# Kernel optimization log

Measured on AMD Instinct MI355X. Metric: run time of the kernel, lower is better.

## Reference

```python
import jax, jax.numpy as jnp
from jax import lax
import numpy as np

B, C, H, W = 32, 64, 128, 128
O, K, KS = 64, 4, 3
HIDDEN = int(C * 0.25) + 1  # 17, per ScaleAwareAttention2d


def setup_inputs() -> dict:
    key = jax.random.key(0)
    ks = jax.random.split(key, 6)
    return {
        "x": jax.random.normal(ks[0], (B, C, H, W), dtype=jnp.float32),
        "scale": jax.random.uniform(ks[1], (1,), dtype=jnp.float32),
        "fc1_w": jax.random.normal(ks[2], (HIDDEN, C), dtype=jnp.float32) * 0.1,
        "fc2_w": jax.random.normal(ks[3], (K, HIDDEN + 2), dtype=jnp.float32) * 0.1,
        "fc2_b": jnp.zeros((K,), dtype=jnp.float32),
        "weight": jax.random.normal(ks[4], (K, O, C, KS, KS), dtype=jnp.float32) * 0.05,
        "bias": jax.random.normal(ks[5], (K, O), dtype=jnp.float32) * 0.05,
    }


def reference(x, scale, fc1_w, fc2_w, fc2_b, weight, bias):
    b = x.shape[0]
    # --- ScaleAwareAttention2d (eval mode -> temperature = 1) ---
    pooled = x.mean(axis=(2, 3))                      # [B, C]  (adaptive avg pool to 1x1)
    h = jax.nn.relu(pooled @ fc1_w.T)                 # [B, HIDDEN]  (1x1 conv, no bias)
    h = jnp.concatenate([h, jnp.ones((b, 2), x.dtype) * scale], axis=1)  # [B, HIDDEN+2]
    logits = h @ fc2_w.T + fc2_b                      # [B, K]
    attn = jax.nn.softmax(logits, axis=1)             # temperature = 1 at inference

    # --- per-sample weight/bias aggregation ---
    agg_w = jnp.einsum('bk,koihw->boihw', attn, weight)  # [B, O, C, KS, KS]
    agg_b = attn @ bias                                   # [B, O]

    # --- per-sample conv (equivalent of F.conv2d with groups = batch) ---
    def one_sample(xi, wi):
        return lax.conv_general_dilated(
            xi[None], wi, window_strides=(1, 1), padding=((1, 1), (1, 1)),
            dimension_numbers=('NCHW', 'OIHW', 'NCHW'))[0]

    out = jax.vmap(one_sample)(x, agg_w)              # [B, O, H, W]
    return out + agg_b[:, :, None, None]
```

## Files before the change

kernel.cpp:

```cpp
#include <hip/hip_runtime.h>
#include <hip/hip_bf16.h>

#define BB 32
#define CC 64
#define HH 128
#define WW 128
#define OO 64
#define KK 4
#define HIDDEN 17
#define HW (HH*WW)

typedef __attribute__((ext_vector_type(8)))  short bf16x8;
typedef __attribute__((ext_vector_type(16))) float f32x16;

typedef __attribute__((address_space(3))) void       lds_void_t;
typedef const __attribute__((address_space(1))) void gbl_void_t;

__device__ __forceinline__ unsigned short f2bf(float f) {
    unsigned u = __float_as_uint(f);
    unsigned r = (u + 0x7FFFu + ((u >> 16) & 1u)) >> 16;
    return (unsigned short)r;
}

__global__ __launch_bounds__(256) void zero_pool_kernel(float* __restrict__ pooled) {
    int i = blockIdx.x * 256 + threadIdx.x;
    if (i < BB * CC) pooled[i] = 0.f;
}

__global__ __launch_bounds__(256) void pool_kernel(const float* __restrict__ x,
                                                   float* __restrict__ pooled) {
    int bc = blockIdx.x;
    const float* p = x + (size_t)bc * HW;
    float s = 0.f;
    for (int i = threadIdx.x; i < HW; i += 256) s += p[i];
    #pragma unroll
    for (int off = 32; off > 0; off >>= 1) s += __shfl_down(s, off, 64);
    __shared__ float warp_s[4];
    int lane = threadIdx.x & 63, wv = threadIdx.x >> 6;
    if (lane == 0) warp_s[wv] = s;
    __syncthreads();
    if (threadIdx.x == 0) {
        float t = warp_s[0] + warp_s[1] + warp_s[2] + warp_s[3];
        pooled[bc] = t * (1.f / (float)HW);
    }
}

__global__ __launch_bounds__(256) void attn_kernel(const float* __restrict__ pooled,
                                                   const float* __restrict__ fc1_w,
                                                   const float* __restrict__ fc2_w,
                                                   const float* __restrict__ fc2_b,
                                                   const float* __restrict__ scale,
                                                   const float* __restrict__ bias,
                                                   float* __restrict__ attn,
                                                   float* __restrict__ agg_b) {
    __shared__ float s_attn[BB * KK];
    int tid = threadIdx.x;
    if (tid < BB) {
        int b = tid;
        const float* pb = pooled + b * CC;
        float h[HIDDEN];
        #pragma unroll
        for (int i = 0; i < HIDDEN; ++i) {
            float s = 0.f;
            for (int c = 0; c < CC; ++c) s += pb[c] * fc1_w[i * CC + c];
            h[i] = fmaxf(s, 0.f);
        }
        float sc = scale[0];
        float logits[KK];
        #pragma unroll
        for (int k = 0; k < KK; ++k) {
            float s = fc2_b[k];
            for (int j = 0; j < HIDDEN; ++j) s += h[j] * fc2_w[k * (HIDDEN + 2) + j];
            s += sc * fc2_w[k * (HIDDEN + 2) + HIDDEN];
            s += sc * fc2_w[k * (HIDDEN + 2) + HIDDEN + 1];
            logits[k] = s;
        }
        float m = fmaxf(fmaxf(logits[0], logits[1]), fmaxf(logits[2], logits[3]));
        float e[KK], tot = 0.f;
        #pragma unroll
        for (int k = 0; k < KK; ++k) { e[k] = __expf(logits[k] - m); tot += e[k]; }
        float inv = 1.f / tot;
        #pragma unroll
        for (int k = 0; k < KK; ++k) {
            float a = e[k] * inv;
            s_attn[b * KK + k] = a;
            attn[b * KK + k] = a;
        }
    }
    __syncthreads();
    for (int i = tid; i < BB * OO; i += blockDim.x) {
        int b = i >> 6;
        int o = i & 63;
        float s = 0.f;
        #pragma unroll
        for (int k = 0; k < KK; ++k) s += s_attn[b * KK + k] * bias[k * OO + o];
        agg_b[i] = s;
    }
}

__global__ __launch_bounds__(256) void aggw_fused_kernel(const float* __restrict__ pooled,
                                                         const float* __restrict__ fc1_w,
                                                         const float* __restrict__ fc2_w,
                                                         const float* __restrict__ fc2_b,
                                                         const float* __restrict__ scale,
                                                         const float* __restrict__ bias,
                                                         const float* __restrict__ weight,
                                                         float* __restrict__ agg_b,
                                                         unsigned int* __restrict__ wbf) {
    __shared__ float4 sw4[128 * 37];
    __shared__ float  sh[4][20];
    __shared__ float  sa[4][4];
    const float* swf = (const float*)sw4;

    const int tid = threadIdx.x;
    const int b4  = blockIdx.x;
    const int oty = blockIdx.y;
    const int kcz = blockIdx.z;

    {
        const float4* w4 = (const float4*)weight;
        #pragma unroll
        for (int it = 0; it < 18; ++it) {
            int i   = tid + it * 256;
            int seg = i / 36;
            int off = i - seg * 36;
            int k   = seg >> 5;
            int o   = seg & 31;
            sw4[seg * 37 + off] = w4[(size_t)(k * 64 + oty * 32 + o) * 144 + kcz * 36 + off];
        }
    }
    const int wv = tid >> 6, lane = tid & 63;
    const int bb = b4 * 4 + wv;
    if (lane < HIDDEN) {
        const float* pb = pooled + bb * CC;
        const float* f1 = fc1_w + lane * CC;
        float s = 0.f;
        #pragma unroll
        for (int c = 0; c < CC; ++c) s += pb[c] * f1[c];
        sh[wv][lane] = fmaxf(s, 0.f);
    }
    __syncthreads();
    if (lane == 0) {
        float sc = scale[0];
        float lg[KK];
        #pragma unroll
        for (int k = 0; k < KK; ++k) {
            float s = fc2_b[k];
            #pragma unroll
            for (int j = 0; j < HIDDEN; ++j) s += sh[wv][j] * fc2_w[k * (HIDDEN + 2) + j];
            s += sc * fc2_w[k * (HIDDEN + 2) + HIDDEN];
            s += sc * fc2_w[k * (HIDDEN + 2) + HIDDEN + 1];
            lg[k] = s;
        }
        float m = fmaxf(fmaxf(lg[0], lg[1]), fmaxf(lg[2], lg[3]));
        float e[KK], tot = 0.f;
        #pragma unroll
        for (int k = 0; k < KK; ++k) { e[k] = __expf(lg[k] - m); tot += e[k]; }
        float inv = 1.f / tot;
        #pragma unroll
        for (int k = 0; k < KK; ++k) sa[wv][k] = e[k] * inv;
    }
    __syncthreads();

    if (oty == 0 && kcz == 0) {
        int bl = tid >> 6, o = tid & 63;
        float s = 0.f;
        #pragma unroll
        for (int k = 0; k < KK; ++k) s += sa[bl][k] * bias[k * OO + o];
        agg_b[(b4 * 4 + bl) * OO + o] = s;
    }

    const int lane6 = tid >> 2;
    const int j2    = tid & 3;
    const int m     = lane6 & 31;
    const int kh2   = lane6 >> 5;
    const int cl    = kh2 * 8 + j2 * 2;
    #pragma unroll
    for (int bl = 0; bl < 4; ++bl) {
        const int b = b4 * 4 + bl;
        const float a0 = sa[bl][0], a1 = sa[bl][1], a2 = sa[bl][2], a3 = sa[bl][3];
        #pragma unroll
        for (int j9 = 0; j9 < 9; ++j9) {
            float s0, s1;
            {
                const float* p0 = swf + (0 * 32 + m) * 148 + cl * 9 + j9;
                const float* p1 = swf + (1 * 32 + m) * 148 + cl * 9 + j9;
                const float* p2 = swf + (2 * 32 + m) * 148 + cl * 9 + j9;
                const float* p3 = swf + (3 * 32 + m) * 148 + cl * 9 + j9;
                s0 = a0 * p0[0] + a1 * p1[0] + a2 * p2[0] + a3 * p3[0];
                s1 = a0 * p0[9] + a1 * p1[9] + a2 * p2[9] + a3 * p3[9];
            }
            wbf[(((size_t)b * 9 + j9) * 8 + oty * 4 + kcz) * 256 + tid] =
                (unsigned int)f2bf(s0) | ((unsigned int)f2bf(s1) << 16);
        }
    }
}

__global__ __launch_bounds__(256) void xpose_pool_kernel(const float* __restrict__ x,
                                                         unsigned int* __restrict__ xbf32,
                                                         float* __restrict__ pooled) {
    __shared__ float t2[64][68];
    __shared__ float s_red[4][64];
    const int y  = blockIdx.x;
    const int b  = blockIdx.y;
    const int x0 = blockIdx.z * 64;
    const int tid = threadIdx.x;
    {
        const int xq = tid & 15;
        const int cb = (tid >> 4) * 4;
        #pragma unroll
        for (int i = 0; i < 4; ++i) {
            const int c = cb + i;
            const float4 v = *(const float4*)(x + (size_t)(b * CC + c) * HW
                                                + (size_t)y * WW + x0 + xq * 4);
            t2[xq * 4 + 0][c] = v.x;
            t2[xq * 4 + 1][c] = v.y;
            t2[xq * 4 + 2][c] = v.z;
            t2[xq * 4 + 3][c] = v.w;
        }
    }
    __syncthreads();
    {
        const int c = tid & 63, q = tid >> 6;
        float s = 0.f;
        #pragma unroll
        for (int i = 0; i < 16; ++i) s += t2[q * 16 + i][c];
        s_red[q][c] = s;
    }
    {
        const int xl  = tid >> 2;
        const int xg  = x0 + xl;
        const int key = (xg + 1) & 7;
        unsigned int* dst = xbf32 + ((size_t)(b * HH + y) * WW + xg) * 32;
        #pragma unroll
        for (int gg = 0; gg < 2; ++gg) {
            const int g = (tid & 3) + gg * 4;
            const float* src = &t2[xl][g * 8];
            uint4 pk;
            pk.x = (unsigned int)f2bf(src[0]) | ((unsigned int)f2bf(src[1]) << 16);
            pk.y = (unsigned int)f2bf(src[2]) | ((unsigned int)f2bf(src[3]) << 16);
            pk.z = (unsigned int)f2bf(src[4]) | ((unsigned int)f2bf(src[5]) << 16);
            pk.w = (unsigned int)f2bf(src[6]) | ((unsigned int)f2bf(src[7]) << 16);
            *(uint4*)(dst + (g ^ key) * 4) = pk;
        }
    }
    __syncthreads();
    if (tid < CC) {
        float s = s_red[0][tid] + s_red[1][tid] + s_red[2][tid] + s_red[3][tid];
        atomicAdd(pooled + b * CC + tid, s * (1.f / (float)HW));
    }
}

#define LROW 16640
__global__ __launch_bounds__(256, 3) void conv_mfma_kernel(const short* __restrict__ xbf,
                                                           const short* __restrict__ wbf,
                                                           const float* __restrict__ agg_b,
                                                           float* __restrict__ out) {
    __shared__ __attribute__((aligned(16))) char ldsbuf[3 * LROW];
    unsigned int* lds32 = (unsigned int*)ldsbuf;

    const int s    = blockIdx.x;
    const int y    = ((s & 7) << 4) | (s >> 3);
    const int b    = blockIdx.y;
    const int tid  = threadIdx.x;
    const int lane = tid & 63;
    const int w    = tid >> 6;

    if (tid < 192) {
        int r = tid / 64;
        int q = tid - r * 64;
        int word = (q < 32) ? (r * (LROW/4) + q)
                            : (r * (LROW/4) + 129 * 32 + (q - 32));
        lds32[word] = 0u;
    }
    {
        const short* growb = xbf + (size_t)b * HH * WW * CC;
        #pragma unroll
        for (int i = 0; i < 12; ++i) {
            int call = w * 12 + i;
            int r   = call >> 4;
            int seg = call & 15;
            int iy  = y - 1 + r;
            if (iy >= 0 && iy < HH) {
                const short* g = growb + (size_t)iy * (WW * CC) + seg * 512 + lane * 8;
                char* lp = ldsbuf + r * LROW + 128 + seg * 1024;
                __builtin_amdgcn_global_load_lds((gbl_void_t*)g, (lds_void_t*)lp, 16, 0, 0);
            }
        }
    }
    if (y == 0)   for (int i = tid; i < 4096; i += 256) lds32[32 + i] = 0u;
    if (y == 127) for (int i = tid; i < 4096; i += 256) lds32[2 * (LROW/4) + 32 + i] = 0u;
    __syncthreads();

    const int otile = w & 1;
    const int o0    = otile * 32;
    const int x0    = (w >> 1) * 64;
    const int m     = lane & 31;
    const int kh2   = lane >> 5;
    const int cbase = kh2 * 16;

    f32x16 acc0 = {0,0,0,0,0,0,0,0,0,0,0,0,0,0,0,0};
    f32x16 acc1 = {0,0,0,0,0,0,0,0,0,0,0,0,0,0,0,0};

    const char* ldsc = ldsbuf;
    #pragma unroll
    for (int j9 = 0; j9 < 9; ++j9) {
        const int kh = j9 / 3, kw = j9 % 3;
        const short* Aj = wbf + (((size_t)b * 9 + j9) * 2 + otile) * 2048 + lane * 8;
        const int p0  = x0 + m + kw;
        const int sw  = ((m + kw) & 7) << 4;
        const int a0b = kh * LROW + p0 * 128;
        const int a1b = a0b + 32 * 128;
        #pragma unroll
        for (int kc = 0; kc < 4; ++kc) {
            bf16x8 a  = *(const bf16x8*)(Aj + kc * 512);
            const int c_off = (cbase + kc * 32) ^ sw;
            bf16x8 b0 = *(const bf16x8*)(ldsc + a0b + c_off);
            bf16x8 b1 = *(const bf16x8*)(ldsc + a1b + c_off);
            acc0 = __builtin_amdgcn_mfma_f32_32x32x16_bf16(a, b0, acc0, 0, 0, 0);
            acc1 = __builtin_amdgcn_mfma_f32_32x32x16_bf16(a, b1, acc1, 0, 0, 0);
        }
    }

    #pragma unroll
    for (int r = 0; r < 16; ++r) {
        int o = o0 + (r & 3) + 8 * (r >> 2) + 4 * kh2;
        float bias = agg_b[b * OO + o];
        size_t base = ((size_t)(b * OO + o) * HH + y) * WW;
        out[base + x0 + m]      = acc0[r] + bias;
        out[base + x0 + 32 + m] = acc1[r] + bias;
    }
}

__global__ __launch_bounds__(256) void aggw_kernel(const float* __restrict__ attn,
                                                   const float* __restrict__ weight,
                                                   float* __restrict__ agg_w) {
    int idx = blockIdx.x * 256 + threadIdx.x;
    const int total = BB * CC * OO * 9;
    if (idx >= total) return;
    int j  = idx % 9;
    int t  = idx / 9;
    int o  = t & 63;
    int t2 = t >> 6;
    int c  = t2 & 63;
    int b  = t2 >> 6;
    float s = 0.f;
    #pragma unroll
    for (int k = 0; k < KK; ++k)
        s += attn[b * KK + k] * weight[((k * OO + o) * CC + c) * 9 + j];
    agg_w[idx] = s;
}

__global__ __launch_bounds__(256) void conv_kernel(const float* __restrict__ x,
                                                   const float* __restrict__ agg_w,
                                                   const float* __restrict__ agg_b,
                                                   float* __restrict__ out) {
    __shared__ float s_in[2][18 * 20];
    const int tid = threadIdx.x;
    const int tx = tid & 15, ty = tid >> 4;
    const int b  = blockIdx.z;
    const int o0 = blockIdx.y * 8;
    const int sy = (blockIdx.x >> 3) * 16;
    const int sx = (blockIdx.x & 7) * 16;

    const float* __restrict__ xb = x + (size_t)b * CC * HW;
    const float* __restrict__ wb = agg_w + (size_t)b * CC * OO * 9;

    float acc[8];
    #pragma unroll
    for (int o = 0; o < 8; ++o) acc[o] = agg_b[b * OO + o0 + o];

    auto load_ch = [&](int c, float* dst) {
        for (int i = tid; i < 18 * 18; i += 256) {
            int r   = i / 18;
            int col = i - r * 18;
            int gy = sy + r - 1;
            int gx = sx + col - 1;
            float v = 0.f;
            if (gy >= 0 && gy < HH && gx >= 0 && gx < WW)
                v = xb[c * HW + gy * WW + gx];
            dst[r * 20 + col] = v;
        }
    };

    load_ch(0, s_in[0]);
    __syncthreads();

    for (int c = 0; c < CC; ++c) {
        const int buf = c & 1;
        if (c + 1 < CC) load_ch(c + 1, s_in[buf ^ 1]);
        float in[3][3];
        #pragma unroll
        for (int kh = 0; kh < 3; ++kh)
            #pragma unroll
            for (int kw = 0; kw < 3; ++kw)
                in[kh][kw] = s_in[buf][(ty + kh) * 20 + (tx + kw)];
        const float* __restrict__ wc = wb + (c * OO + o0) * 9;
        #pragma unroll
        for (int o = 0; o < 8; ++o)
            #pragma unroll
            for (int kh = 0; kh < 3; ++kh)
                #pragma unroll
                for (int kw = 0; kw < 3; ++kw)
                    acc[o] += in[kh][kw] * wc[o * 9 + kh * 3 + kw];
        __syncthreads();
    }

    const int oy = sy + ty, ox = sx + tx;
    #pragma unroll
    for (int o = 0; o < 8; ++o)
        out[((size_t)(b * OO + o0 + o) * HH + oy) * WW + ox] = acc[o];
}

extern "C" void kernel_launch(void* const* d_in, const int* in_sizes, int n_in,
                              void* d_out, int out_size, void* d_ws, size_t ws_size,
                              hipStream_t stream) {
    const float* x      = (const float*)d_in[0];
    const float* scale  = (const float*)d_in[1];
    const float* fc1_w  = (const float*)d_in[2];
    const float* fc2_w  = (const float*)d_in[3];
    const float* fc2_b  = (const float*)d_in[4];
    const float* weight = (const float*)d_in[5];
    const float* bias   = (const float*)d_in[6];
    float* out = (float*)d_out;

    const size_t XBF_BYTES = (size_t)BB * HH * WW * CC * 2;
    const size_t WBF_BYTES = (size_t)BB * 9 * OO * CC * 2;
    const size_t NEED = XBF_BYTES + WBF_BYTES + (2048 + 128 + 2048) * 4 + 256;

    if (ws_size >= NEED) {
        short*        xbf   = (short*)d_ws;
        unsigned int* xbf32 = (unsigned int*)d_ws;
        unsigned int* wbf32 = (unsigned int*)((char*)d_ws + XBF_BYTES);
        short*        wbf   = (short*)wbf32;
        float*        fls   = (float*)((char*)d_ws + XBF_BYTES + WBF_BYTES);
        float* pooled = fls;
        float* agg_b  = fls + 2048 + 128;

        zero_pool_kernel<<<8, 256, 0, stream>>>(pooled);
        xpose_pool_kernel<<<dim3(HH, BB, 2), 256, 0, stream>>>(x, xbf32, pooled);
        aggw_fused_kernel<<<dim3(8, 2, 4), 256, 0, stream>>>(pooled, fc1_w, fc2_w, fc2_b,
                                                             scale, bias, weight, agg_b, wbf32);
        conv_mfma_kernel<<<dim3(HH, BB), 256, 0, stream>>>(xbf, wbf, agg_b, out);
    } else {
        float* ws     = (float*)d_ws;
        float* attn   = ws;
        float* agg_b  = ws + 128;
        float* pooled = ws + 128 + 2048;
        float* agg_w  = ws + 128 + 2048 + 2048;
        pool_kernel<<<BB * CC, 256, 0, stream>>>(x, pooled);
        attn_kernel<<<1, 256, 0, stream>>>(pooled, fc1_w, fc2_w, fc2_b, scale, bias, attn, agg_b);
        const int aggw_total = BB * CC * OO * 9;
        aggw_kernel<<<(aggw_total + 255) / 256, 256, 0, stream>>>(attn, weight, agg_w);
        conv_kernel<<<dim3(64, 8, BB), 256, 0, stream>>>(x, agg_w, agg_b, out);
    }
}
```

Measured before the change: 301.4 us.

## Compute two output rows per conv block to reuse weight fragments and halo rows

The MFMA conv kernel now handles two output rows per block, loading four input rows into LDS instead of three, and each weight fragment feeds four MFMAs instead of two. This cuts redundant halo-row loads and global weight reads per output row, and halves the grid. In exchange it uses more LDS and accumulator registers and lowers occupancy to 2 blocks per CU, with fewer blocks available to hide latency.

```diff
diff --git a/kernel.cpp b/kernel.cpp
--- a/kernel.cpp
+++ b/kernel.cpp
@@ -252,23 +252,24 @@
 }
 
 #define LROW 16640
-__global__ __launch_bounds__(256, 3) void conv_mfma_kernel(const short* __restrict__ xbf,
+__global__ __launch_bounds__(256, 2) void conv_mfma_kernel(const short* __restrict__ xbf,
                                                            const short* __restrict__ wbf,
                                                            const float* __restrict__ agg_b,
                                                            float* __restrict__ out) {
-    __shared__ __attribute__((aligned(16))) char ldsbuf[3 * LROW];
+    __shared__ __attribute__((aligned(16))) char ldsbuf[4 * LROW];
     unsigned int* lds32 = (unsigned int*)ldsbuf;
 
     const int s    = blockIdx.x;
-    const int y    = ((s & 7) << 4) | (s >> 3);
+    const int Y    = ((s & 7) << 3) | (s >> 3);
+    const int y0   = Y * 2;
     const int b    = blockIdx.y;
     const int tid  = threadIdx.x;
     const int lane = tid & 63;
     const int w    = tid >> 6;
 
-    if (tid < 192) {
-        int r = tid / 64;
-        int q = tid - r * 64;
+    {
+        int r = tid >> 6;
+        int q = tid & 63;
         int word = (q < 32) ? (r * (LROW/4) + q)
                             : (r * (LROW/4) + 129 * 32 + (q - 32));
         lds32[word] = 0u;
@@ -276,11 +277,11 @@
     {
         const short* growb = xbf + (size_t)b * HH * WW * CC;
         #pragma unroll
-        for (int i = 0; i < 12; ++i) {
-            int call = w * 12 + i;
+        for (int i = 0; i < 16; ++i) {
+            int call = w * 16 + i;
             int r   = call >> 4;
             int seg = call & 15;
-            int iy  = y - 1 + r;
+            int iy  = y0 - 1 + r;
             if (iy >= 0 && iy < HH) {
                 const short* g = growb + (size_t)iy * (WW * CC) + seg * 512 + lane * 8;
                 char* lp = ldsbuf + r * LROW + 128 + seg * 1024;
@@ -288,8 +289,8 @@
             }
         }
     }
-    if (y == 0)   for (int i = tid; i < 4096; i += 256) lds32[32 + i] = 0u;
-    if (y == 127) for (int i = tid; i < 4096; i += 256) lds32[2 * (LROW/4) + 32 + i] = 0u;
+    if (Y == 0)  for (int i = tid; i < 4096; i += 256) lds32[32 + i] = 0u;
+    if (Y == 63) for (int i = tid; i < 4096; i += 256) lds32[3 * (LROW/4) + 32 + i] = 0u;
     __syncthreads();
 
     const int otile = w & 1;
@@ -299,8 +300,10 @@
     const int kh2   = lane >> 5;
     const int cbase = kh2 * 16;
 
-    f32x16 acc0 = {0,0,0,0,0,0,0,0,0,0,0,0,0,0,0,0};
-    f32x16 acc1 = {0,0,0,0,0,0,0,0,0,0,0,0,0,0,0,0};
+    f32x16 acc00 = {0,0,0,0,0,0,0,0,0,0,0,0,0,0,0,0};
+    f32x16 acc01 = {0,0,0,0,0,0,0,0,0,0,0,0,0,0,0,0};
+    f32x16 acc10 = {0,0,0,0,0,0,0,0,0,0,0,0,0,0,0,0};
+    f32x16 acc11 = {0,0,0,0,0,0,0,0,0,0,0,0,0,0,0,0};
 
     const char* ldsc = ldsbuf;
     #pragma unroll
@@ -309,16 +312,19 @@
         const short* Aj = wbf + (((size_t)b * 9 + j9) * 2 + otile) * 2048 + lane * 8;
         const int p0  = x0 + m + kw;
         const int sw  = ((m + kw) & 7) << 4;
-        const int a0b = kh * LROW + p0 * 128;
-        const int a1b = a0b + 32 * 128;
         #pragma unroll
         for (int kc = 0; kc < 4; ++kc) {
-            bf16x8 a  = *(const bf16x8*)(Aj + kc * 512);
+            bf16x8 a = *(const bf16x8*)(Aj + kc * 512);
             const int c_off = (cbase + kc * 32) ^ sw;
-            bf16x8 b0 = *(const bf16x8*)(ldsc + a0b + c_off);
-            bf16x8 b1 = *(const bf16x8*)(ldsc + a1b + c_off);
-            acc0 = __builtin_amdgcn_mfma_f32_32x32x16_bf16(a, b0, acc0, 0, 0, 0);
-            acc1 = __builtin_amdgcn_mfma_f32_32x32x16_bf16(a, b1, acc1, 0, 0, 0);
+            const int base0 = kh * LROW + p0 * 128 + c_off;
+            bf16x8 b00 = *(const bf16x8*)(ldsc + base0);
+            bf16x8 b01 = *(const bf16x8*)(ldsc + base0 + 32 * 128);
+            bf16x8 b10 = *(const bf16x8*)(ldsc + base0 + LROW);
+            bf16x8 b11 = *(const bf16x8*)(ldsc + base0 + LROW + 32 * 128);
+            acc00 = __builtin_amdgcn_mfma_f32_32x32x16_bf16(a, b00, acc00, 0, 0, 0);
+            acc01 = __builtin_amdgcn_mfma_f32_32x32x16_bf16(a, b01, acc01, 0, 0, 0);
+            acc10 = __builtin_amdgcn_mfma_f32_32x32x16_bf16(a, b10, acc10, 0, 0, 0);
+            acc11 = __builtin_amdgcn_mfma_f32_32x32x16_bf16(a, b11, acc11, 0, 0, 0);
         }
     }
 
@@ -326,9 +332,11 @@
     for (int r = 0; r < 16; ++r) {
         int o = o0 + (r & 3) + 8 * (r >> 2) + 4 * kh2;
         float bias = agg_b[b * OO + o];
-        size_t base = ((size_t)(b * OO + o) * HH + y) * WW;
-        out[base + x0 + m]      = acc0[r] + bias;
-        out[base + x0 + 32 + m] = acc1[r] + bias;
+        size_t base = ((size_t)(b * OO + o) * HH + y0) * WW;
+        out[base + x0 + m]           = acc00[r] + bias;
+        out[base + x0 + 32 + m]      = acc01[r] + bias;
+        out[base + WW + x0 + m]      = acc10[r] + bias;
+        out[base + WW + x0 + 32 + m] = acc11[r] + bias;
     }
 }
 
@@ -441,7 +449,7 @@
         xpose_pool_kernel<<<dim3(HH, BB, 2), 256, 0, stream>>>(x, xbf32, pooled);
         aggw_fused_kernel<<<dim3(8, 2, 4), 256, 0, stream>>>(pooled, fc1_w, fc2_w, fc2_b,
                                                              scale, bias, weight, agg_b, wbf32);
-        conv_mfma_kernel<<<dim3(HH, BB), 256, 0, stream>>>(xbf, wbf, agg_b, out);
+        conv_mfma_kernel<<<dim3(64, BB), 256, 0, stream>>>(xbf, wbf, agg_b, out);
     } else {
         float* ws     = (float*)d_ws;
         float* attn   = ws;
```

Measured after the change: 305.3 us. About the same (+1.3%).

## Process eight output rows per conv block with a rotating LDS row ring

Applied to the files above, without the earlier changes.

Each conv block now computes eight consecutive output rows instead of one. It keeps the 9x4 weight fragments in registers across rows and streams input rows through a 4-slot LDS ring, prefetching the next row while the current one is computed. This removes the 3x re-fetch of halo rows and the per-row weight reloads, and it seeds the accumulators with the bias. The costs are fewer blocks (16x32 instead of 128x32), lower occupancy (2 waves per SIMD) and more registers, which could reduce latency hiding.

```diff
diff --git a/kernel.cpp b/kernel.cpp
--- a/kernel.cpp
+++ b/kernel.cpp
@@ -252,44 +252,50 @@
 }
 
 #define LROW 16640
-__global__ __launch_bounds__(256, 3) void conv_mfma_kernel(const short* __restrict__ xbf,
+#define NY 8
+__global__ __launch_bounds__(256, 2) void conv_mfma_kernel(const short* __restrict__ xbf,
                                                            const short* __restrict__ wbf,
                                                            const float* __restrict__ agg_b,
                                                            float* __restrict__ out) {
-    __shared__ __attribute__((aligned(16))) char ldsbuf[3 * LROW];
+    __shared__ __attribute__((aligned(16))) char ldsbuf[4 * LROW];
     unsigned int* lds32 = (unsigned int*)ldsbuf;
 
-    const int s    = blockIdx.x;
-    const int y    = ((s & 7) << 4) | (s >> 3);
+    const int Ycl  = blockIdx.x;
+    const int y0   = Ycl * NY;
     const int b    = blockIdx.y;
     const int tid  = threadIdx.x;
     const int lane = tid & 63;
     const int w    = tid >> 6;
 
-    if (tid < 192) {
-        int r = tid / 64;
-        int q = tid - r * 64;
-        int word = (q < 32) ? (r * (LROW/4) + q)
-                            : (r * (LROW/4) + 129 * 32 + (q - 32));
+    {
+        int r = tid >> 6;
+        int q = tid & 63;
+        int word = (q < 32) ? (r * (LROW / 4) + q)
+                            : (r * (LROW / 4) + 129 * 32 + (q - 32));
         lds32[word] = 0u;
     }
-    {
-        const short* growb = xbf + (size_t)b * HH * WW * CC;
-        #pragma unroll
-        for (int i = 0; i < 12; ++i) {
-            int call = w * 12 + i;
-            int r   = call >> 4;
-            int seg = call & 15;
-            int iy  = y - 1 + r;
-            if (iy >= 0 && iy < HH) {
-                const short* g = growb + (size_t)iy * (WW * CC) + seg * 512 + lane * 8;
-                char* lp = ldsbuf + r * LROW + 128 + seg * 1024;
-                __builtin_amdgcn_global_load_lds((gbl_void_t*)g, (lds_void_t*)lp, 16, 0, 0);
-            }
-        }
-    }
-    if (y == 0)   for (int i = tid; i < 4096; i += 256) lds32[32 + i] = 0u;
-    if (y == 127) for (int i = tid; i < 4096; i += 256) lds32[2 * (LROW/4) + 32 + i] = 0u;
+
+    const short* growb = xbf + (size_t)b * HH * WW * CC;
+
+    auto stage4 = [&](int row, int slot) {
+        const short* g = growb + (size_t)row * (WW * CC);
+        #pragma unroll
+        for (int i = 0; i < 4; ++i) {
+            int seg = w * 4 + i;
+            const short* gp = g + seg * 512 + lane * 8;
+            char* lp = ldsbuf + slot * LROW + 128 + seg * 1024;
+            __builtin_amdgcn_global_load_lds((gbl_void_t*)gp, (lds_void_t*)lp, 16, 0, 0);
+        }
+    };
+    auto zero_slot = [&](int slot) {
+        uint4* p = (uint4*)(ldsbuf + slot * LROW + 128);
+        #pragma unroll
+        for (int i = 0; i < 4; ++i) p[tid + i * 256] = make_uint4(0u, 0u, 0u, 0u);
+    };
+
+    if (y0 - 1 >= 0) stage4(y0 - 1, 0); else zero_slot(0);
+    stage4(y0,     1);
+    stage4(y0 + 1, 2);
     __syncthreads();
 
     const int otile = w & 1;
@@ -299,36 +305,62 @@
     const int kh2   = lane >> 5;
     const int cbase = kh2 * 16;
 
-    f32x16 acc0 = {0,0,0,0,0,0,0,0,0,0,0,0,0,0,0,0};
-    f32x16 acc1 = {0,0,0,0,0,0,0,0,0,0,0,0,0,0,0,0};
-
-    const char* ldsc = ldsbuf;
+    bf16x8 A[9][4];
     #pragma unroll
     for (int j9 = 0; j9 < 9; ++j9) {
-        const int kh = j9 / 3, kw = j9 % 3;
         const short* Aj = wbf + (((size_t)b * 9 + j9) * 2 + otile) * 2048 + lane * 8;
-        const int p0  = x0 + m + kw;
-        const int sw  = ((m + kw) & 7) << 4;
-        const int a0b = kh * LROW + p0 * 128;
-        const int a1b = a0b + 32 * 128;
-        #pragma unroll
-        for (int kc = 0; kc < 4; ++kc) {
-            bf16x8 a  = *(const bf16x8*)(Aj + kc * 512);
-            const int c_off = (cbase + kc * 32) ^ sw;
-            bf16x8 b0 = *(const bf16x8*)(ldsc + a0b + c_off);
-            bf16x8 b1 = *(const bf16x8*)(ldsc + a1b + c_off);
-            acc0 = __builtin_amdgcn_mfma_f32_32x32x16_bf16(a, b0, acc0, 0, 0, 0);
-            acc1 = __builtin_amdgcn_mfma_f32_32x32x16_bf16(a, b1, acc1, 0, 0, 0);
-        }
-    }
-
-    #pragma unroll
-    for (int r = 0; r < 16; ++r) {
-        int o = o0 + (r & 3) + 8 * (r >> 2) + 4 * kh2;
-        float bias = agg_b[b * OO + o];
-        size_t base = ((size_t)(b * OO + o) * HH + y) * WW;
-        out[base + x0 + m]      = acc0[r] + bias;
-        out[base + x0 + 32 + m] = acc1[r] + bias;
+        #pragma unroll
+        for (int kc = 0; kc < 4; ++kc) A[j9][kc] = *(const bf16x8*)(Aj + kc * 512);
+    }
+    float biasv[16];
+    #pragma unroll
+    for (int r = 0; r < 16; ++r)
+        biasv[r] = agg_b[b * OO + o0 + (r & 3) + 8 * (r >> 2) + 4 * kh2];
+
+    for (int iy = 0; iy < NY; ++iy) {
+        asm volatile("s_waitcnt lgkmcnt(0)" ::: "memory");
+        __builtin_amdgcn_s_barrier();
+        bool did = false;
+        if (iy < NY - 1) {
+            const int row = y0 + iy + 2;
+            const int slot = (iy + 3) & 3;
+            if (row < HH) { stage4(row, slot); did = true; }
+            else          zero_slot(slot);
+        }
+        if (did) asm volatile("s_waitcnt vmcnt(4) lgkmcnt(0)" ::: "memory");
+        else     asm volatile("s_waitcnt vmcnt(0) lgkmcnt(0)" ::: "memory");
+        __builtin_amdgcn_s_barrier();
+        __builtin_amdgcn_sched_barrier(0);
+
+        f32x16 acc0, acc1;
+        #pragma unroll
+        for (int r = 0; r < 16; ++r) { acc0[r] = biasv[r]; acc1[r] = biasv[r]; }
+
+        #pragma unroll
+        for (int j9 = 0; j9 < 9; ++j9) {
+            const int kh = j9 / 3, kw = j9 % 3;
+            const int slot = (iy + kh) & 3;
+            const int p0 = x0 + m + kw;
+            const int sw = ((m + kw) & 7) << 4;
+            const int base0 = slot * LROW + p0 * 128;
+            #pragma unroll
+            for (int kc = 0; kc < 4; ++kc) {
+                const int c_off = (cbase + kc * 32) ^ sw;
+                bf16x8 b0 = *(const bf16x8*)(ldsbuf + base0 + c_off);
+                bf16x8 b1 = *(const bf16x8*)(ldsbuf + base0 + 32 * 128 + c_off);
+                acc0 = __builtin_amdgcn_mfma_f32_32x32x16_bf16(A[j9][kc], b0, acc0, 0, 0, 0);
+                acc1 = __builtin_amdgcn_mfma_f32_32x32x16_bf16(A[j9][kc], b1, acc1, 0, 0, 0);
+            }
+        }
+
+        const int y = y0 + iy;
+        #pragma unroll
+        for (int r = 0; r < 16; ++r) {
+            int o = o0 + (r & 3) + 8 * (r >> 2) + 4 * kh2;
+            size_t base = ((size_t)(b * OO + o) * HH + y) * WW;
+            out[base + x0 + m]      = acc0[r];
+            out[base + x0 + 32 + m] = acc1[r];
+        }
     }
 }
 
@@ -441,7 +473,7 @@
         xpose_pool_kernel<<<dim3(HH, BB, 2), 256, 0, stream>>>(x, xbf32, pooled);
         aggw_fused_kernel<<<dim3(8, 2, 4), 256, 0, stream>>>(pooled, fc1_w, fc2_w, fc2_b,
                                                              scale, bias, weight, agg_b, wbf32);
-        conv_mfma_kernel<<<dim3(HH, BB), 256, 0, stream>>>(xbf, wbf, agg_b, out);
+        conv_mfma_kernel<<<dim3(16, BB), 256, 0, stream>>>(xbf, wbf, agg_b, out);
     } else {
         float* ws     = (float*)d_ws;
         float* attn   = ws;
```

After: 299.4 us. Within noise of the previous version (-0.7%).
